# Kernel optimization log

Measured on AMD Instinct MI355X. Metric: run time of the kernel, lower is better.

The kernel has to match this reference:

```python
import jax, jax.numpy as jnp
import numpy as np

ASSIGN_RATIO = 0.1  # hard-coded inside coarsen_graph in the original
EPS_CUT = 1e-7
EPS_NORM = 1e-12  # torch F.normalize eps


def _normalize_batch_adj(adj):
    # adj: [B, N, N]
    n = adj.shape[1]
    A = adj + jnp.eye(n, dtype=adj.dtype)
    deg_inv_sqrt = jnp.clip(A.sum(-1), 1.0, None) ** -0.5  # [B, N]
    newA = deg_inv_sqrt[..., :, None] * A * deg_inv_sqrt[..., None, :]
    row_mask = (adj.sum(-1) > 0).astype(adj.dtype)  # [B, N]
    return row_mask[..., :, None] * newA


def setup_inputs():
    key = jax.random.key(0)
    k0, k1, k2, k3, k4 = jax.random.split(key, 5)
    B, N, D, T = 512, 128, 256, 512
    concept_hidden = jax.random.normal(k0, (B, N, D), jnp.float32)
    adj = jax.random.uniform(k1, (B, N, N), jnp.float32)
    head = jax.random.randint(k2, (B, T), 0, N)
    lin_w = jax.random.normal(k3, (1, D), jnp.float32) / np.sqrt(D).astype(np.float32)
    bias = jax.random.normal(k4, (1,), jnp.float32)
    return {"concept_hidden": concept_hidden, "adj": adj, "head": head,
            "lin_w": lin_w, "bias": bias}


def reference(concept_hidden, adj, head, lin_w, bias):
    # concept_hidden: [B, N, D], adj: [B, N, N], head: [B, T] node indices
    x = concept_hidden
    B, N, D = x.shape

    out = x @ lin_w.T                      # [B, N, 1]  self.lin(x)
    norm_adj = _normalize_batch_adj(adj)   # [B, N, N]
    out = norm_adj @ out + bias            # [B, N, 1]
    alpha = jax.nn.sigmoid(out ** 2)[..., 0]  # [B, N]

    # batch_num_nodes[i] = len(set(head[i]))  -> count unique via sort
    hs = jnp.sort(head, axis=-1)
    n_uniq = 1 + (hs[:, 1:] != hs[:, :-1]).sum(-1)  # [B]

    # per-sample k = ceil(n * 0.1) + 1 (only when n > 1); cut = k-th largest alpha
    k = jnp.ceil(n_uniq.astype(jnp.float32) * ASSIGN_RATIO).astype(jnp.int32) + 1
    a_desc = jnp.sort(alpha, axis=-1)[:, ::-1]       # descending
    idx = jnp.clip(k - 1, 0, N - 1)
    cut = jnp.take_along_axis(a_desc, idx[:, None], axis=-1)[:, 0]
    cut = jnp.where(n_uniq > 1, cut, jnp.zeros_like(cut))  # [B]

    cut_alpha = jax.nn.relu(alpha + EPS_CUT - cut[:, None])  # [B, N]

    # S = norm_adj * cut_alpha broadcast over rows, then L1-normalize rows
    S = norm_adj * cut_alpha[:, None, :]
    S = S / jnp.clip(jnp.abs(S).sum(-1, keepdims=True), EPS_NORM, None)

    St = jnp.swapaxes(S, 1, 2)             # [B, N, N]
    embedding_tensor = St @ x              # S^T x   [B, N, D]
    new_adj = (St @ adj) @ S               # S^T A S [B, N, N]
    return embedding_tensor, new_adj
```

## Files before the change

kernel.cpp:

```cpp
#include <hip/hip_runtime.h>

#define Bsz 512
#define Nn  128
#define Dd  256
#define Tt  512

typedef __attribute__((ext_vector_type(8))) short short8;
typedef __attribute__((ext_vector_type(4))) float f32x4;

__device__ __forceinline__ ushort f2bf(float f) {
    union { float f; unsigned u; } v; v.f = f;
    unsigned r = v.u + 0x7fffu + ((v.u >> 16) & 1u);
    return (ushort)(r >> 16);
}
__device__ __forceinline__ unsigned pk2(float a, float b) {
    return (unsigned)f2bf(a) | ((unsigned)f2bf(b) << 16);
}
__device__ __forceinline__ short8 pk8(const float* v) {
    union { uint4 u; short8 s; } c;
    c.u.x = pk2(v[0], v[1]); c.u.y = pk2(v[2], v[3]);
    c.u.z = pk2(v[4], v[5]); c.u.w = pk2(v[6], v[7]);
    return c.s;
}

__global__ __launch_bounds__(1024) void mega(
    const float* __restrict__ x, const float* __restrict__ adj,
    const int* __restrict__ head, const float* __restrict__ lin_w,
    const float* __restrict__ bias,
    float* __restrict__ emb, float* __restrict__ nadj)
{
    const int b = blockIdx.x, t = threadIdx.x;
    __shared__ __align__(16) float bufA[Nn][132];
    __shared__ __align__(16) ushort STl[Nn][136];
    __shared__ float wS[Dd];
    __shared__ float ttS[Nn], disS[Nn], maskS[Nn], alphaS[Nn], uS[Nn], rowcS[Nn];
    __shared__ float partS[Nn][9];
    __shared__ float dotP[Nn][9];
    __shared__ int   flags[Nn];
    __shared__ int   nuniq;
    __shared__ float cutS;

    const float bias0 = bias[0];
    if (t < Dd) wS[t] = lin_w[t];
    if (t < Nn) flags[t] = 0;
    if (t == 0) { nuniq = 0; cutS = 0.f; }

    const float* adjb = adj + (size_t)b * Nn * Nn;
#pragma unroll
    for (int i = 0; i < 4; ++i) {
        int f = t + 1024 * i;
        int rr = f >> 5, c = (f & 31) * 4;
        *(float4*)&bufA[rr][c] = *(const float4*)&adjb[(size_t)rr * Nn + c];
    }
    __syncthreads();

    if (t < Tt) { int h = head[(size_t)b * Tt + t]; flags[h] = 1; }

    {
        const int dr = t >> 3, dh = t & 7;
        const float4* xr = (const float4*)(x + ((size_t)b * Nn + dr) * Dd + dh * 32);
        float p = 0.f;
#pragma unroll
        for (int i = 0; i < 8; ++i) {
            float4 v = xr[i];
            const float* w = &wS[dh * 32 + 4 * i];
            p += v.x * w[0] + v.y * w[1] + v.z * w[2] + v.w * w[3];
        }
        dotP[dr][dh] = p;
    }

    const int r = t >> 3, seg = t & 7, cbs = seg * 16;
    {
        float4 s4 = {0.f, 0.f, 0.f, 0.f};
#pragma unroll
        for (int j = 0; j < 4; ++j) {
            float4 v = *(float4*)&bufA[r][cbs + 4 * j];
            s4.x += v.x; s4.y += v.y; s4.z += v.z; s4.w += v.w;
        }
        partS[r][seg] = (s4.x + s4.y) + (s4.z + s4.w);
    }
    __syncthreads();

    if (t < Nn) {
        float rs = 0.f, dt = 0.f;
#pragma unroll
        for (int j = 0; j < 8; ++j) { rs += partS[t][j]; dt += dotP[t][j]; }
        maskS[t]  = (rs > 0.f) ? 1.f : 0.f;
        float dis = 1.f / sqrtf(fmaxf(rs + 1.f, 1.f));
        disS[t]   = dis;
        ttS[t]    = dis * dt;
        atomicAdd(&nuniq, flags[t]);
    }
    __syncthreads();

    {
        float4 a = {0.f, 0.f, 0.f, 0.f};
#pragma unroll
        for (int j = 0; j < 4; ++j) {
            float4 v = *(float4*)&bufA[r][cbs + 4 * j];
            float4 w = *(float4*)&ttS[cbs + 4 * j];
            a.x += v.x * w.x; a.y += v.y * w.y; a.z += v.z * w.z; a.w += v.w * w.w;
        }
        partS[r][seg] = (a.x + a.y) + (a.z + a.w);
    }
    __syncthreads();
    if (t < Nn) {
        float mv = 0.f;
#pragma unroll
        for (int j = 0; j < 8; ++j) mv += partS[t][j];
        float o = maskS[t] * disS[t] * (mv + ttS[t]) + bias0;
        alphaS[t] = 1.f / (1.f + expf(-o * o));
    }
    __syncthreads();
    if (t < Nn) {
        int nu = nuniq;
        if (nu > 1) {
            int idx = (int)ceilf((float)nu * 0.1f);
            if (idx > Nn - 1) idx = Nn - 1;
            float an = alphaS[t];
            int cg = 0, ce = 0;
            for (int j = 0; j < Nn; ++j) {
                float aj = alphaS[j];
                cg += (aj > an); ce += (aj == an);
            }
            if (cg <= idx && idx < cg + ce) cutS = an;
        }
    }
    __syncthreads();
    if (t < Nn) uS[t] = fmaxf(alphaS[t] + 1e-7f - cutS, 0.f) * disS[t];
    __syncthreads();
    {
        float4 a = {0.f, 0.f, 0.f, 0.f};
#pragma unroll
        for (int j = 0; j < 4; ++j) {
            float4 v = *(float4*)&bufA[r][cbs + 4 * j];
            float4 w = *(float4*)&uS[cbs + 4 * j];
            a.x += v.x * w.x; a.y += v.y * w.y; a.z += v.z * w.z; a.w += v.w * w.w;
        }
        partS[r][seg] = (a.x + a.y) + (a.z + a.w);
    }
    __syncthreads();
    if (t < Nn) {
        float tot = uS[t];
#pragma unroll
        for (int j = 0; j < 8; ++j) tot += partS[t][j];
        float rsum = maskS[t] * disS[t] * tot;
        rowcS[t]   = maskS[t] * disS[t] / fmaxf(rsum, 1e-12f);
    }
    __syncthreads();

    {
        const int m = t & 127, sl = t >> 7, k0 = sl * 16;
        const float um = uS[m];
        float vv[16];
#pragma unroll
        for (int j = 0; j < 16; ++j) {
            int k = k0 + j;
            vv[j] = rowcS[k] * (bufA[k][m] + ((k == m) ? 1.f : 0.f)) * um;
        }
        uint4 p0, p1;
        p0.x = pk2(vv[0],  vv[1]);  p0.y = pk2(vv[2],  vv[3]);
        p0.z = pk2(vv[4],  vv[5]);  p0.w = pk2(vv[6],  vv[7]);
        p1.x = pk2(vv[8],  vv[9]);  p1.y = pk2(vv[10], vv[11]);
        p1.z = pk2(vv[12], vv[13]); p1.w = pk2(vv[14], vv[15]);
        *(uint4*)&STl[m][k0]     = p0;
        *(uint4*)&STl[m][k0 + 8] = p1;
    }
    __syncthreads();

    const int lane = t & 63, w = t >> 6;
    const int l15 = lane & 15, quad = lane >> 4;
    const int mrow  = (w & 7) * 16;
    const int nhalf = (w >> 3) * 64;
    f32x4 acc[4];

#pragma unroll
    for (int nt = 0; nt < 4; ++nt) acc[nt] = (f32x4){0.f, 0.f, 0.f, 0.f};
#pragma unroll
    for (int k0 = 0; k0 < 128; k0 += 32) {
        float av[8];
        *(float4*)&av[0] = *(float4*)&bufA[mrow + l15][k0 + quad * 8];
        *(float4*)&av[4] = *(float4*)&bufA[mrow + l15][k0 + quad * 8 + 4];
        short8 a0 = pk8(av);
#pragma unroll
        for (int nt = 0; nt < 4; ++nt) {
            short8 bf = *(const short8*)&STl[nhalf + nt * 16 + l15][k0 + quad * 8];
            acc[nt] = __builtin_amdgcn_mfma_f32_16x16x32_bf16(a0, bf, acc[nt], 0, 0, 0);
        }
    }
    __syncthreads();

    ushort (*PT)[136] = (ushort(*)[136])&bufA[0][0];
#pragma unroll
    for (int nt = 0; nt < 4; ++nt) {
        int j    = nhalf + nt * 16 + l15;
        int mcol = mrow + quad * 4;
        uint2 wv2;
        wv2.x = pk2(acc[nt][0], acc[nt][1]);
        wv2.y = pk2(acc[nt][2], acc[nt][3]);
        *(uint2*)&PT[j][mcol] = wv2;
    }
    __syncthreads();

#pragma unroll
    for (int nt = 0; nt < 4; ++nt) acc[nt] = (f32x4){0.f, 0.f, 0.f, 0.f};
#pragma unroll
    for (int k0 = 0; k0 < 128; k0 += 32) {
        short8 a0 = *(const short8*)&STl[mrow + l15][k0 + quad * 8];
#pragma unroll
        for (int nt = 0; nt < 4; ++nt) {
            short8 bf = *(const short8*)&PT[nhalf + nt * 16 + l15][k0 + quad * 8];
            acc[nt] = __builtin_amdgcn_mfma_f32_16x16x32_bf16(a0, bf, acc[nt], 0, 0, 0);
        }
    }
#pragma unroll
    for (int nt = 0; nt < 4; ++nt)
#pragma unroll
        for (int rr = 0; rr < 4; ++rr) {
            int row = mrow + quad * 4 + rr;
            int col = nhalf + nt * 16 + l15;
            nadj[((size_t)b * Nn + row) * Nn + col] = acc[nt][rr];
        }
    __syncthreads();

    float (*xbufK)[65] = (float(*)[65])&bufA[0][0];
    short8 aE[4];
#pragma unroll
    for (int ks = 0; ks < 4; ++ks)
        aE[ks] = *(const short8*)&STl[mrow + l15][ks * 32 + quad * 8];
    const int dcb = (w >> 3) * 32;

    for (int qd = 0; qd < 4; ++qd) {
        const int d0 = qd * 64;
#pragma unroll
        for (int i = 0; i < 2; ++i) {
            int f = t + 1024 * i;
            int k = f >> 4, c4 = (f & 15) * 4;
            float4 v = *(const float4*)&x[((size_t)b * Nn + k) * Dd + d0 + c4];
            xbufK[k][c4]     = v.x; xbufK[k][c4 + 1] = v.y;
            xbufK[k][c4 + 2] = v.z; xbufK[k][c4 + 3] = v.w;
        }
        __syncthreads();
        f32x4 accE[2];
        accE[0] = (f32x4){0.f, 0.f, 0.f, 0.f};
        accE[1] = (f32x4){0.f, 0.f, 0.f, 0.f};
#pragma unroll
        for (int ks = 0; ks < 4; ++ks) {
#pragma unroll
            for (int s = 0; s < 2; ++s) {
                const int dcol = dcb + s * 16;
                float bv[8];
#pragma unroll
                for (int j = 0; j < 8; ++j)
                    bv[j] = xbufK[ks * 32 + quad * 8 + j][dcol + l15];
                short8 bf = pk8(bv);
                accE[s] = __builtin_amdgcn_mfma_f32_16x16x32_bf16(aE[ks], bf, accE[s], 0, 0, 0);
            }
        }
#pragma unroll
        for (int s = 0; s < 2; ++s)
#pragma unroll
            for (int rr = 0; rr < 4; ++rr) {
                int row = mrow + quad * 4 + rr;
                int col = d0 + dcb + s * 16 + l15;
                emb[((size_t)b * Nn + row) * Dd + col] = accE[s][rr];
            }
        __syncthreads();
    }
}

extern "C" void kernel_launch(void* const* d_in, const int* in_sizes, int n_in,
                              void* d_out, int out_size, void* d_ws, size_t ws_size,
                              hipStream_t stream)
{
    const float* x     = (const float*)d_in[0];
    const float* adj   = (const float*)d_in[1];
    const int*   head  = (const int*)d_in[2];
    const float* lin_w = (const float*)d_in[3];
    const float* bias  = (const float*)d_in[4];

    float* emb  = (float*)d_out;
    float* nadj = emb + (size_t)Bsz * Nn * Dd;

    mega<<<Bsz, 1024, 0, stream>>>(x, adj, head, lin_w, bias, emb, nadj);
}
```

Baseline: 214.4 us.

## Store adj as bf16 in LDS and stage x transposed bf16-packed for MFMA

Converts adj to bf16 once on load, so shared-memory footprint shrinks and the first GEMM reads ready-made bf16 fragments. The x tile for the embedding GEMM is staged as transposed packed bf16 pairs in two 128-column halves instead of four 64-column float quarters, replacing per-element gathers and packing with vector loads. It also drops the lin_w LDS copy, uses 512 threads for the projection dot, and sets a min-blocks hint in launch_bounds. The trade-off is that degree sums and alpha now come from bf16-rounded adj, which lowers precision in the cut selection.

```diff
diff --git a/kernel.cpp b/kernel.cpp
--- a/kernel.cpp
+++ b/kernel.cpp
@@ -16,32 +16,27 @@
 __device__ __forceinline__ unsigned pk2(float a, float b) {
     return (unsigned)f2bf(a) | ((unsigned)f2bf(b) << 16);
 }
-__device__ __forceinline__ short8 pk8(const float* v) {
-    union { uint4 u; short8 s; } c;
-    c.u.x = pk2(v[0], v[1]); c.u.y = pk2(v[2], v[3]);
-    c.u.z = pk2(v[4], v[5]); c.u.w = pk2(v[6], v[7]);
-    return c.s;
-}
-
-__global__ __launch_bounds__(1024) void mega(
+__device__ __forceinline__ float bf2f(ushort u) {
+    union { unsigned u; float f; } v; v.u = (unsigned)u << 16; return v.f;
+}
+
+__global__ __launch_bounds__(1024, 8) void mega(
     const float* __restrict__ x, const float* __restrict__ adj,
     const int* __restrict__ head, const float* __restrict__ lin_w,
     const float* __restrict__ bias,
     float* __restrict__ emb, float* __restrict__ nadj)
 {
     const int b = blockIdx.x, t = threadIdx.x;
-    __shared__ __align__(16) float bufA[Nn][132];
+    __shared__ __align__(16) ushort adjB[Nn][136];
     __shared__ __align__(16) ushort STl[Nn][136];
-    __shared__ float wS[Dd];
     __shared__ float ttS[Nn], disS[Nn], maskS[Nn], alphaS[Nn], uS[Nn], rowcS[Nn];
     __shared__ float partS[Nn][9];
-    __shared__ float dotP[Nn][9];
+    __shared__ float dotP[Nn][4];
     __shared__ int   flags[Nn];
     __shared__ int   nuniq;
     __shared__ float cutS;
 
     const float bias0 = bias[0];
-    if (t < Dd) wS[t] = lin_w[t];
     if (t < Nn) flags[t] = 0;
     if (t == 0) { nuniq = 0; cutS = 0.f; }
 
@@ -50,41 +45,43 @@
     for (int i = 0; i < 4; ++i) {
         int f = t + 1024 * i;
         int rr = f >> 5, c = (f & 31) * 4;
-        *(float4*)&bufA[rr][c] = *(const float4*)&adjb[(size_t)rr * Nn + c];
+        float4 v = *(const float4*)&adjb[(size_t)rr * Nn + c];
+        uint2 w2; w2.x = pk2(v.x, v.y); w2.y = pk2(v.z, v.w);
+        *(uint2*)&adjB[rr][c] = w2;
     }
     __syncthreads();
 
     if (t < Tt) { int h = head[(size_t)b * Tt + t]; flags[h] = 1; }
 
-    {
-        const int dr = t >> 3, dh = t & 7;
-        const float4* xr = (const float4*)(x + ((size_t)b * Nn + dr) * Dd + dh * 32);
+    if (t < 512) {
+        const int dr = t >> 2, dh = t & 3;
+        const float4* xr = (const float4*)(x + ((size_t)b * Nn + dr) * Dd + dh * 64);
+        const float4* wr = (const float4*)(lin_w + dh * 64);
         float p = 0.f;
 #pragma unroll
-        for (int i = 0; i < 8; ++i) {
-            float4 v = xr[i];
-            const float* w = &wS[dh * 32 + 4 * i];
-            p += v.x * w[0] + v.y * w[1] + v.z * w[2] + v.w * w[3];
+        for (int i = 0; i < 16; ++i) {
+            float4 v = xr[i], w4 = wr[i];
+            p += v.x * w4.x + v.y * w4.y + v.z * w4.z + v.w * w4.w;
         }
         dotP[dr][dh] = p;
     }
 
-    const int r = t >> 3, seg = t & 7, cbs = seg * 16;
-    {
-        float4 s4 = {0.f, 0.f, 0.f, 0.f};
-#pragma unroll
-        for (int j = 0; j < 4; ++j) {
-            float4 v = *(float4*)&bufA[r][cbs + 4 * j];
-            s4.x += v.x; s4.y += v.y; s4.z += v.z; s4.w += v.w;
-        }
-        partS[r][seg] = (s4.x + s4.y) + (s4.z + s4.w);
-    }
-    __syncthreads();
-
-    if (t < Nn) {
-        float rs = 0.f, dt = 0.f;
-#pragma unroll
-        for (int j = 0; j < 8; ++j) { rs += partS[t][j]; dt += dotP[t][j]; }
+    const int r = t >> 3, seg = t & 7;
+    {
+        short8 a0 = *(const short8*)&adjB[r][seg * 16];
+        short8 a1 = *(const short8*)&adjB[r][seg * 16 + 8];
+        float s = 0.f;
+#pragma unroll
+        for (int j = 0; j < 8; ++j) s += bf2f((ushort)a0[j]) + bf2f((ushort)a1[j]);
+        partS[r][seg] = s;
+    }
+    __syncthreads();
+
+    if (t < Nn) {
+        float rs = 0.f;
+#pragma unroll
+        for (int j = 0; j < 8; ++j) rs += partS[t][j];
+        float dt = dotP[t][0] + dotP[t][1] + dotP[t][2] + dotP[t][3];
         maskS[t]  = (rs > 0.f) ? 1.f : 0.f;
         float dis = 1.f / sqrtf(fmaxf(rs + 1.f, 1.f));
         disS[t]   = dis;
@@ -94,14 +91,15 @@
     __syncthreads();
 
     {
-        float4 a = {0.f, 0.f, 0.f, 0.f};
-#pragma unroll
-        for (int j = 0; j < 4; ++j) {
-            float4 v = *(float4*)&bufA[r][cbs + 4 * j];
-            float4 w = *(float4*)&ttS[cbs + 4 * j];
-            a.x += v.x * w.x; a.y += v.y * w.y; a.z += v.z * w.z; a.w += v.w * w.w;
-        }
-        partS[r][seg] = (a.x + a.y) + (a.z + a.w);
+        short8 a0 = *(const short8*)&adjB[r][seg * 16];
+        short8 a1 = *(const short8*)&adjB[r][seg * 16 + 8];
+        float s = 0.f;
+#pragma unroll
+        for (int j = 0; j < 8; ++j) {
+            s += bf2f((ushort)a0[j]) * ttS[seg * 16 + j];
+            s += bf2f((ushort)a1[j]) * ttS[seg * 16 + 8 + j];
+        }
+        partS[r][seg] = s;
     }
     __syncthreads();
     if (t < Nn) {
@@ -130,14 +128,15 @@
     if (t < Nn) uS[t] = fmaxf(alphaS[t] + 1e-7f - cutS, 0.f) * disS[t];
     __syncthreads();
     {
-        float4 a = {0.f, 0.f, 0.f, 0.f};
-#pragma unroll
-        for (int j = 0; j < 4; ++j) {
-            float4 v = *(float4*)&bufA[r][cbs + 4 * j];
-            float4 w = *(float4*)&uS[cbs + 4 * j];
-            a.x += v.x * w.x; a.y += v.y * w.y; a.z += v.z * w.z; a.w += v.w * w.w;
-        }
-        partS[r][seg] = (a.x + a.y) + (a.z + a.w);
+        short8 a0 = *(const short8*)&adjB[r][seg * 16];
+        short8 a1 = *(const short8*)&adjB[r][seg * 16 + 8];
+        float s = 0.f;
+#pragma unroll
+        for (int j = 0; j < 8; ++j) {
+            s += bf2f((ushort)a0[j]) * uS[seg * 16 + j];
+            s += bf2f((ushort)a1[j]) * uS[seg * 16 + 8 + j];
+        }
+        partS[r][seg] = s;
     }
     __syncthreads();
     if (t < Nn) {
@@ -156,7 +155,7 @@
 #pragma unroll
         for (int j = 0; j < 16; ++j) {
             int k = k0 + j;
-            vv[j] = rowcS[k] * (bufA[k][m] + ((k == m) ? 1.f : 0.f)) * um;
+            vv[j] = rowcS[k] * (bf2f(adjB[k][m]) + ((k == m) ? 1.f : 0.f)) * um;
         }
         uint4 p0, p1;
         p0.x = pk2(vv[0],  vv[1]);  p0.y = pk2(vv[2],  vv[3]);
@@ -178,10 +177,7 @@
     for (int nt = 0; nt < 4; ++nt) acc[nt] = (f32x4){0.f, 0.f, 0.f, 0.f};
 #pragma unroll
     for (int k0 = 0; k0 < 128; k0 += 32) {
-        float av[8];
-        *(float4*)&av[0] = *(float4*)&bufA[mrow + l15][k0 + quad * 8];
-        *(float4*)&av[4] = *(float4*)&bufA[mrow + l15][k0 + quad * 8 + 4];
-        short8 a0 = pk8(av);
+        short8 a0 = *(const short8*)&adjB[mrow + l15][k0 + quad * 8];
 #pragma unroll
         for (int nt = 0; nt < 4; ++nt) {
             short8 bf = *(const short8*)&STl[nhalf + nt * 16 + l15][k0 + quad * 8];
@@ -190,15 +186,15 @@
     }
     __syncthreads();
 
-    ushort (*PT)[136] = (ushort(*)[136])&bufA[0][0];
+    ushort (*PT)[136] = (ushort(*)[136])&adjB[0][0];
 #pragma unroll
     for (int nt = 0; nt < 4; ++nt) {
         int j    = nhalf + nt * 16 + l15;
         int mcol = mrow + quad * 4;
-        uint2 wv2;
-        wv2.x = pk2(acc[nt][0], acc[nt][1]);
-        wv2.y = pk2(acc[nt][2], acc[nt][3]);
-        *(uint2*)&PT[j][mcol] = wv2;
+        uint2 w2;
+        w2.x = pk2(acc[nt][0], acc[nt][1]);
+        w2.y = pk2(acc[nt][2], acc[nt][3]);
+        *(uint2*)&PT[j][mcol] = w2;
     }
     __syncthreads();
 
@@ -223,47 +219,46 @@
         }
     __syncthreads();
 
-    float (*xbufK)[65] = (float(*)[65])&bufA[0][0];
+    uint (*xTp)[68] = (uint(*)[68])&adjB[0][0];
     short8 aE[4];
 #pragma unroll
     for (int ks = 0; ks < 4; ++ks)
         aE[ks] = *(const short8*)&STl[mrow + l15][ks * 32 + quad * 8];
-    const int dcb = (w >> 3) * 32;
-
-    for (int qd = 0; qd < 4; ++qd) {
-        const int d0 = qd * 64;
+    const int dcb = (w >> 3) * 64;
+
+    for (int half = 0; half < 2; ++half) {
+        const int d0 = half * 128;
 #pragma unroll
         for (int i = 0; i < 2; ++i) {
             int f = t + 1024 * i;
-            int k = f >> 4, c4 = (f & 15) * 4;
-            float4 v = *(const float4*)&x[((size_t)b * Nn + k) * Dd + d0 + c4];
-            xbufK[k][c4]     = v.x; xbufK[k][c4 + 1] = v.y;
-            xbufK[k][c4 + 2] = v.z; xbufK[k][c4 + 3] = v.w;
+            int d4 = f & 31, kp = f >> 5;
+            const float* xp = x + ((size_t)b * Nn + 2 * kp) * Dd + d0 + 4 * d4;
+            float4 ve = *(const float4*)xp;
+            float4 vo = *(const float4*)(xp + Dd);
+            xTp[4 * d4    ][kp] = pk2(ve.x, vo.x);
+            xTp[4 * d4 + 1][kp] = pk2(ve.y, vo.y);
+            xTp[4 * d4 + 2][kp] = pk2(ve.z, vo.z);
+            xTp[4 * d4 + 3][kp] = pk2(ve.w, vo.w);
         }
         __syncthreads();
-        f32x4 accE[2];
-        accE[0] = (f32x4){0.f, 0.f, 0.f, 0.f};
-        accE[1] = (f32x4){0.f, 0.f, 0.f, 0.f};
+        f32x4 accE[4];
+#pragma unroll
+        for (int nt = 0; nt < 4; ++nt) accE[nt] = (f32x4){0.f, 0.f, 0.f, 0.f};
 #pragma unroll
         for (int ks = 0; ks < 4; ++ks) {
 #pragma unroll
-            for (int s = 0; s < 2; ++s) {
-                const int dcol = dcb + s * 16;
-                float bv[8];
-#pragma unroll
-                for (int j = 0; j < 8; ++j)
-                    bv[j] = xbufK[ks * 32 + quad * 8 + j][dcol + l15];
-                short8 bf = pk8(bv);
-                accE[s] = __builtin_amdgcn_mfma_f32_16x16x32_bf16(aE[ks], bf, accE[s], 0, 0, 0);
+            for (int nt = 0; nt < 4; ++nt) {
+                short8 bf = *(const short8*)&xTp[dcb + nt * 16 + l15][ks * 16 + quad * 4];
+                accE[nt] = __builtin_amdgcn_mfma_f32_16x16x32_bf16(aE[ks], bf, accE[nt], 0, 0, 0);
             }
         }
 #pragma unroll
-        for (int s = 0; s < 2; ++s)
+        for (int nt = 0; nt < 4; ++nt)
 #pragma unroll
             for (int rr = 0; rr < 4; ++rr) {
                 int row = mrow + quad * 4 + rr;
-                int col = d0 + dcb + s * 16 + l15;
-                emb[((size_t)b * Nn + row) * Dd + col] = accE[s][rr];
+                int col = d0 + dcb + nt * 16 + l15;
+                emb[((size_t)b * Nn + row) * Dd + col] = accE[nt][rr];
             }
         __syncthreads();
     }
```

Result: faster. 200.2 us (-6.6%).
